# Kernel tuning notes

Measured on AMD Instinct MI355X. Metric: run time of the kernel, lower is better.

The kernel has to match this reference:

```python
import jax, jax.numpy as jnp
import numpy as np

D_IN, D_HID = 64, 128

def _ff(x, w1, b1, w2, b2):
    # FeedForward: Linear -> ReLU -> Linear
    return jax.nn.relu(x @ w1 + b1) @ w2 + b2

def setup_inputs() -> dict:
    key = jax.random.key(0)
    ks = jax.random.split(key, 10)
    N, m = 8, 2048
    def lin(k, fan_in, fan_out):
        bound = 1.0 / np.sqrt(fan_in)
        return jax.random.uniform(k, (fan_in, fan_out), jnp.float32, -bound, bound)
    return {
        "x": jax.random.normal(ks[0], (N, m, D_IN), jnp.float32),
        "edge": jax.random.uniform(ks[1], (N, m, m), jnp.float32),
        # f: dim_in -> dim_hid//2 -> dim_hid
        "f_w1": lin(ks[2], D_IN, D_HID // 2),
        "f_b1": jnp.zeros((D_HID // 2,), jnp.float32),
        "f_w2": lin(ks[3], D_HID // 2, D_HID),
        "f_b2": jnp.zeros((D_HID,), jnp.float32),
        # g: 2*dim_in -> dim_hid -> dim_hid
        "g_w1": lin(ks[4], 2 * D_IN, D_HID),
        "g_b1": jnp.zeros((D_HID,), jnp.float32),
        "g_w2": lin(ks[5], D_HID, D_HID),
        "g_b2": jnp.zeros((D_HID,), jnp.float32),
    }

def reference(x, edge, f_w1, f_b1, f_w2, f_b2, g_w1, g_b1, g_w2, g_b2):
    # self dynamics: f(x) -> [N, m, D_HID]
    self_dyn = _ff(x, f_w1, f_b1, f_w2, f_b2)
    # Original builds interaction[n,i,j] = cat(x[n,i], x[n,i]) (receiver is
    # transposed twice), so g is constant along j. Compute g once per sender node.
    gx = _ff(jnp.concatenate([x, x], axis=-1), g_w1, g_b1, g_w2, g_b2)  # [N, m, H]
    # interaction.sum over sender dim i with edge weights: out[n,j] = sum_i edge[n,i,j]*gx[n,i]
    inter = jnp.einsum('nij,nih->njh', edge, gx)
    return self_dyn + inter
```

## Files before the change

### kernel.cpp

```cpp
#include <hip/hip_runtime.h>


typedef __attribute__((ext_vector_type(8))) short bf16x8;
typedef __attribute__((ext_vector_type(8))) unsigned short u16x8;
typedef __attribute__((ext_vector_type(4))) unsigned short u16x4;
typedef __attribute__((ext_vector_type(4))) float f32x4;

static __device__ __forceinline__ unsigned short f2bf(float f) {
  union { float f; unsigned int i; } c; c.f = f;
  return (unsigned short)((c.i + 0x7fffu + ((c.i >> 16) & 1u)) >> 16);
}

__global__ __launch_bounds__(256) void k_self(
    const float* __restrict__ x,
    const float* __restrict__ fw1,
    const float* __restrict__ fb1,
    const float* __restrict__ fw2,
    const float* __restrict__ fb2,
    float* __restrict__ out)
{
  __shared__ short xs[64 * 64];
  __shared__ short w1T[64 * 64];
  __shared__ short w2T[128 * 64];
  __shared__ short h1s[64 * 64];

  const int t = threadIdx.x;
  const int R0 = blockIdx.x * 64;

  for (int idx = t; idx < 64 * 64; idx += 256) {
    int k = idx >> 6, n = idx & 63;
    w1T[(n << 6) + (((k >> 3) ^ (n & 7)) << 3) + (k & 7)] = (short)f2bf(fw1[idx]);
  }
  for (int idx = t; idx < 64 * 128; idx += 256) {
    int k = idx >> 7, n = idx & 127;
    w2T[(n << 6) + (((k >> 3) ^ (n & 7)) << 3) + (k & 7)] = (short)f2bf(fw2[idx]);
  }
  for (int s = t; s < 64 * 16; s += 256) {
    int row = s >> 4, c4 = s & 15;
    f32x4 v = *(const f32x4*)(x + (size_t)(R0 + row) * 64 + c4 * 4);
    u16x4 pk;
#pragma unroll
    for (int r = 0; r < 4; ++r) pk[r] = f2bf(v[r]);
    *(u16x4*)(xs + (row << 6) + (((c4 >> 1) ^ (row & 7)) << 3) + ((c4 & 1) << 2)) = pk;
  }
  __syncthreads();

  const int w = t >> 6, l = t & 63;
  const int lr = l & 15, q = l >> 4;
  const int mrow = w * 16 + lr;

  bf16x8 a[2];
#pragma unroll
  for (int ks = 0; ks < 2; ++ks) {
    int c = ks * 4 + q;
    a[ks] = *(const bf16x8*)(xs + (mrow << 6) + ((c ^ (mrow & 7)) << 3));
  }

  f32x4 acc;
#pragma unroll
  for (int nf = 0; nf < 4; ++nf) {
    acc = (f32x4){0.f, 0.f, 0.f, 0.f};
#pragma unroll
    for (int ks = 0; ks < 2; ++ks) {
      int c = ks * 4 + q;
      int nr = nf * 16 + lr;
      bf16x8 b = *(const bf16x8*)(w1T + (nr << 6) + ((c ^ (nr & 7)) << 3));
      acc = __builtin_amdgcn_mfma_f32_16x16x32_bf16(a[ks], b, acc, 0, 0, 0);
    }
    float bias = fb1[nf * 16 + lr];
#pragma unroll
    for (int r = 0; r < 4; ++r) {
      float v = acc[r] + bias;
      v = v > 0.f ? v : 0.f;
      int row = w * 16 + q * 4 + r, n = nf * 16 + lr;
      h1s[(row << 6) + (((n >> 3) ^ (row & 7)) << 3) + (n & 7)] = (short)f2bf(v);
    }
  }
  __syncthreads();

  bf16x8 a2[2];
#pragma unroll
  for (int ks = 0; ks < 2; ++ks) {
    int c = ks * 4 + q;
    a2[ks] = *(const bf16x8*)(h1s + (mrow << 6) + ((c ^ (mrow & 7)) << 3));
  }
#pragma unroll
  for (int nf = 0; nf < 8; ++nf) {
    acc = (f32x4){0.f, 0.f, 0.f, 0.f};
#pragma unroll
    for (int ks = 0; ks < 2; ++ks) {
      int c = ks * 4 + q;
      int nr = nf * 16 + lr;
      bf16x8 b = *(const bf16x8*)(w2T + (nr << 6) + ((c ^ (nr & 7)) << 3));
      acc = __builtin_amdgcn_mfma_f32_16x16x32_bf16(a2[ks], b, acc, 0, 0, 0);
    }
    float bias = fb2[nf * 16 + lr];
#pragma unroll
    for (int r = 0; r < 4; ++r)
      out[(size_t)(R0 + w * 16 + q * 4 + r) * 128 + nf * 16 + lr] = acc[r] + bias;
  }
}

__global__ __launch_bounds__(256) void k_gx(
    const float* __restrict__ x,
    const float* __restrict__ gw1,
    const float* __restrict__ gb1,
    const float* __restrict__ gw2,
    const float* __restrict__ gb2,
    unsigned short* __restrict__ gxT)
{
  __shared__ short xs[64 * 64];
  __shared__ short w1T[128 * 64];
  __shared__ short w2T[128 * 128];
  __shared__ short h2s[64 * 128];

  const int t = threadIdx.x;
  const int R0 = blockIdx.x * 64;

  for (int idx = t; idx < 64 * 128; idx += 256) {
    int k = idx >> 7, n = idx & 127;
    float v = gw1[idx] + gw1[64 * 128 + idx];
    w1T[(n << 6) + (((k >> 3) ^ (n & 7)) << 3) + (k & 7)] = (short)f2bf(v);
  }
  for (int idx = t; idx < 128 * 128; idx += 256) {
    int k = idx >> 7, n = idx & 127;
    w2T[(n << 7) + (((k >> 3) ^ (n & 7)) << 3) + (k & 7)] = (short)f2bf(gw2[idx]);
  }
  for (int s = t; s < 64 * 16; s += 256) {
    int row = s >> 4, c4 = s & 15;
    f32x4 v = *(const f32x4*)(x + (size_t)(R0 + row) * 64 + c4 * 4);
    u16x4 pk;
#pragma unroll
    for (int r = 0; r < 4; ++r) pk[r] = f2bf(v[r]);
    *(u16x4*)(xs + (row << 6) + (((c4 >> 1) ^ (row & 7)) << 3) + ((c4 & 1) << 2)) = pk;
  }
  __syncthreads();

  const int w = t >> 6, l = t & 63;
  const int lr = l & 15, q = l >> 4;
  const int mrow = w * 16 + lr;

  bf16x8 a[2];
#pragma unroll
  for (int ks = 0; ks < 2; ++ks) {
    int c = ks * 4 + q;
    a[ks] = *(const bf16x8*)(xs + (mrow << 6) + ((c ^ (mrow & 7)) << 3));
  }

  f32x4 acc;
#pragma unroll
  for (int nf = 0; nf < 8; ++nf) {
    acc = (f32x4){0.f, 0.f, 0.f, 0.f};
#pragma unroll
    for (int ks = 0; ks < 2; ++ks) {
      int c = ks * 4 + q;
      int nr = nf * 16 + lr;
      bf16x8 b = *(const bf16x8*)(w1T + (nr << 6) + ((c ^ (nr & 7)) << 3));
      acc = __builtin_amdgcn_mfma_f32_16x16x32_bf16(a[ks], b, acc, 0, 0, 0);
    }
    float bias = gb1[nf * 16 + lr];
#pragma unroll
    for (int r = 0; r < 4; ++r) {
      float v = acc[r] + bias;
      v = v > 0.f ? v : 0.f;
      int row = w * 16 + q * 4 + r, n = nf * 16 + lr;
      h2s[(row << 7) + (((n >> 3) ^ (row & 7)) << 3) + (n & 7)] = (short)f2bf(v);
    }
  }
  __syncthreads();

  bf16x8 a2[4];
#pragma unroll
  for (int ks = 0; ks < 4; ++ks) {
    int c = ks * 4 + q;
    a2[ks] = *(const bf16x8*)(h2s + (mrow << 7) + ((c ^ (mrow & 7)) << 3));
  }
  const int batch = R0 >> 11;
  const int ib = R0 & 2047;
#pragma unroll
  for (int nf = 0; nf < 8; ++nf) {
    acc = (f32x4){0.f, 0.f, 0.f, 0.f};
#pragma unroll
    for (int ks = 0; ks < 4; ++ks) {
      int c = ks * 4 + q;
      int nr = nf * 16 + lr;
      bf16x8 b = *(const bf16x8*)(w2T + (nr << 7) + ((c ^ (nr & 7)) << 3));
      acc = __builtin_amdgcn_mfma_f32_16x16x32_bf16(a2[ks], b, acc, 0, 0, 0);
    }
    float bias = gb2[nf * 16 + lr];
    u16x4 pk;
#pragma unroll
    for (int r = 0; r < 4; ++r) pk[r] = f2bf(acc[r] + bias);
    *(u16x4*)(gxT + (size_t)(batch * 128 + nf * 16 + lr) * 2048 + ib + w * 16 + q * 4) = pk;
  }
}

typedef __attribute__((ext_vector_type(8))) float f32x8;

__device__ __forceinline__ void load_tiles(const float* eb, const unsigned short* gb,
                                           int i0, int j0, int e_ii, int e_cj,
                                           f32x8 er[2], u16x8 gr[4])
{
  er[0] = *(const f32x8*)(eb + (size_t)(i0 + e_ii) * 2048 + j0 + e_cj * 8);
  er[1] = *(const f32x8*)(eb + (size_t)(i0 + e_ii + 32) * 2048 + j0 + e_cj * 8);
#pragma unroll
  for (int qq = 0; qq < 4; ++qq)
    gr[qq] = *(const u16x8*)(gb + (size_t)(qq * 32 + e_ii) * 2048 + i0 + e_cj * 8);
}

__global__ __launch_bounds__(256) void k_einsum(
    const float* __restrict__ edge,
    const unsigned short* __restrict__ gxT,
    float* __restrict__ out)
{
  __shared__ short eT[64 * 72];
  __shared__ short bT[128 * 64];

  const int t = threadIdx.x;
  const int batch = blockIdx.x & 7;
  const int jt = blockIdx.x >> 3;
  const int j0 = jt * 64;

  const int w = t >> 6, l = t & 63;
  const int wm = w & 1, wn = w >> 1;
  const int lr = l & 15, q = l >> 4;

  const float* eb = edge + (size_t)batch * 2048 * 2048;
  const unsigned short* gb = gxT + (size_t)batch * 128 * 2048;

  const int e_ii = t >> 3;
  const int e_cj = t & 7;

  f32x4 acc[2][4];
#pragma unroll
  for (int f = 0; f < 2; ++f)
#pragma unroll
    for (int nf = 0; nf < 4; ++nf) acc[f][nf] = (f32x4){0.f, 0.f, 0.f, 0.f};

  f32x8 er[2];
  u16x8 gr[4];
  load_tiles(eb, gb, 0, j0, e_ii, e_cj, er, gr);

  for (int kk = 0; kk < 32; ++kk) {
    __syncthreads();
#pragma unroll
    for (int rr = 0; rr < 2; ++rr) {
      int ii = e_ii + rr * 32;
#pragma unroll
      for (int u = 0; u < 8; ++u)
        eT[(e_cj * 8 + u) * 72 + (((ii >> 3) ^ e_cj) << 3) + (ii & 7)] = (short)f2bf(er[rr][u]);
    }
#pragma unroll
    for (int qq = 0; qq < 4; ++qq) {
      int r = qq * 32 + e_ii;
      *(u16x8*)(bT + (r << 6) + ((e_cj ^ (r & 7)) << 3)) = gr[qq];
    }
    __syncthreads();
    if (kk < 31) load_tiles(eb, gb, (kk + 1) * 64, j0, e_ii, e_cj, er, gr);

#pragma unroll
    for (int ks = 0; ks < 2; ++ks) {
      bf16x8 a[2], b[4];
#pragma unroll
      for (int f = 0; f < 2; ++f) {
        int jj = wm * 32 + f * 16 + lr;
        int c = ks * 4 + q;
        a[f] = *(const bf16x8*)(eT + jj * 72 + ((c ^ (jj >> 3)) << 3));
      }
#pragma unroll
      for (int nf = 0; nf < 4; ++nf) {
        int h = wn * 64 + nf * 16 + lr;
        int c = ks * 4 + q;
        b[nf] = *(const bf16x8*)(bT + (h << 6) + ((c ^ (h & 7)) << 3));
      }
#pragma unroll
      for (int f = 0; f < 2; ++f)
#pragma unroll
        for (int nf = 0; nf < 4; ++nf)
          acc[f][nf] = __builtin_amdgcn_mfma_f32_16x16x32_bf16(a[f], b[nf], acc[f][nf], 0, 0, 0);
    }
  }

  const size_t rowbase = (size_t)batch * 2048 + j0 + wm * 32;
#pragma unroll
  for (int f = 0; f < 2; ++f) {
#pragma unroll
    for (int nf = 0; nf < 4; ++nf) {
      int h = wn * 64 + nf * 16 + lr;
#pragma unroll
      for (int r = 0; r < 4; ++r) {
        size_t o = (rowbase + f * 16 + q * 4 + r) * 128 + h;
        out[o] = acc[f][nf][r] + out[o];
      }
    }
  }
}

extern "C" void kernel_launch(void* const* d_in, const int* in_sizes, int n_in,
                              void* d_out, int out_size, void* d_ws, size_t ws_size,
                              hipStream_t stream) {
  const float* x    = (const float*)d_in[0];
  const float* edge = (const float*)d_in[1];
  const float* fw1  = (const float*)d_in[2];
  const float* fb1  = (const float*)d_in[3];
  const float* fw2  = (const float*)d_in[4];
  const float* fb2  = (const float*)d_in[5];
  const float* gw1  = (const float*)d_in[6];
  const float* gb1  = (const float*)d_in[7];
  const float* gw2  = (const float*)d_in[8];
  const float* gb2  = (const float*)d_in[9];
  float* out = (float*)d_out;

  unsigned short* gxT = (unsigned short*)d_ws;

  hipLaunchKernelGGL(k_self, dim3(256), dim3(256), 0, stream, x, fw1, fb1, fw2, fb2, out);
  hipLaunchKernelGGL(k_gx, dim3(256), dim3(256), 0, stream, x, gw1, gb1, gw2, gb2, gxT);
  hipLaunchKernelGGL(k_einsum, dim3(256), dim3(256), 0, stream, edge, gxT, out);
}
```

Measured before the change: 243.7 us.

## Fuse self-dynamics MLP into einsum kernel and halve j-tile to 32

Removes the separate self-dynamics kernel and computes f(x) in the epilogue of the edge-weighted einsum kernel. The second layer accumulates directly into the einsum accumulators, so the out read-modify-write and one launch go away. The j-tile shrinks from 64 to 32 rows, doubling the grid to 512 blocks for better CU occupancy. The cost is that each block reloads the gxT tiles, roughly doubling gxT traffic, and converts the f weights once per block.

```diff
diff --git a/kernel.cpp b/kernel.cpp
--- a/kernel.cpp
+++ b/kernel.cpp
@@ -5,100 +5,11 @@
 typedef __attribute__((ext_vector_type(8))) unsigned short u16x8;
 typedef __attribute__((ext_vector_type(4))) unsigned short u16x4;
 typedef __attribute__((ext_vector_type(4))) float f32x4;
+typedef __attribute__((ext_vector_type(8))) float f32x8;
 
 static __device__ __forceinline__ unsigned short f2bf(float f) {
   union { float f; unsigned int i; } c; c.f = f;
   return (unsigned short)((c.i + 0x7fffu + ((c.i >> 16) & 1u)) >> 16);
-}
-
-__global__ __launch_bounds__(256) void k_self(
-    const float* __restrict__ x,
-    const float* __restrict__ fw1,
-    const float* __restrict__ fb1,
-    const float* __restrict__ fw2,
-    const float* __restrict__ fb2,
-    float* __restrict__ out)
-{
-  __shared__ short xs[64 * 64];
-  __shared__ short w1T[64 * 64];
-  __shared__ short w2T[128 * 64];
-  __shared__ short h1s[64 * 64];
-
-  const int t = threadIdx.x;
-  const int R0 = blockIdx.x * 64;
-
-  for (int idx = t; idx < 64 * 64; idx += 256) {
-    int k = idx >> 6, n = idx & 63;
-    w1T[(n << 6) + (((k >> 3) ^ (n & 7)) << 3) + (k & 7)] = (short)f2bf(fw1[idx]);
-  }
-  for (int idx = t; idx < 64 * 128; idx += 256) {
-    int k = idx >> 7, n = idx & 127;
-    w2T[(n << 6) + (((k >> 3) ^ (n & 7)) << 3) + (k & 7)] = (short)f2bf(fw2[idx]);
-  }
-  for (int s = t; s < 64 * 16; s += 256) {
-    int row = s >> 4, c4 = s & 15;
-    f32x4 v = *(const f32x4*)(x + (size_t)(R0 + row) * 64 + c4 * 4);
-    u16x4 pk;
-#pragma unroll
-    for (int r = 0; r < 4; ++r) pk[r] = f2bf(v[r]);
-    *(u16x4*)(xs + (row << 6) + (((c4 >> 1) ^ (row & 7)) << 3) + ((c4 & 1) << 2)) = pk;
-  }
-  __syncthreads();
-
-  const int w = t >> 6, l = t & 63;
-  const int lr = l & 15, q = l >> 4;
-  const int mrow = w * 16 + lr;
-
-  bf16x8 a[2];
-#pragma unroll
-  for (int ks = 0; ks < 2; ++ks) {
-    int c = ks * 4 + q;
-    a[ks] = *(const bf16x8*)(xs + (mrow << 6) + ((c ^ (mrow & 7)) << 3));
-  }
-
-  f32x4 acc;
-#pragma unroll
-  for (int nf = 0; nf < 4; ++nf) {
-    acc = (f32x4){0.f, 0.f, 0.f, 0.f};
-#pragma unroll
-    for (int ks = 0; ks < 2; ++ks) {
-      int c = ks * 4 + q;
-      int nr = nf * 16 + lr;
-      bf16x8 b = *(const bf16x8*)(w1T + (nr << 6) + ((c ^ (nr & 7)) << 3));
-      acc = __builtin_amdgcn_mfma_f32_16x16x32_bf16(a[ks], b, acc, 0, 0, 0);
-    }
-    float bias = fb1[nf * 16 + lr];
-#pragma unroll
-    for (int r = 0; r < 4; ++r) {
-      float v = acc[r] + bias;
-      v = v > 0.f ? v : 0.f;
-      int row = w * 16 + q * 4 + r, n = nf * 16 + lr;
-      h1s[(row << 6) + (((n >> 3) ^ (row & 7)) << 3) + (n & 7)] = (short)f2bf(v);
-    }
-  }
-  __syncthreads();
-
-  bf16x8 a2[2];
-#pragma unroll
-  for (int ks = 0; ks < 2; ++ks) {
-    int c = ks * 4 + q;
-    a2[ks] = *(const bf16x8*)(h1s + (mrow << 6) + ((c ^ (mrow & 7)) << 3));
-  }
-#pragma unroll
-  for (int nf = 0; nf < 8; ++nf) {
-    acc = (f32x4){0.f, 0.f, 0.f, 0.f};
-#pragma unroll
-    for (int ks = 0; ks < 2; ++ks) {
-      int c = ks * 4 + q;
-      int nr = nf * 16 + lr;
-      bf16x8 b = *(const bf16x8*)(w2T + (nr << 6) + ((c ^ (nr & 7)) << 3));
-      acc = __builtin_amdgcn_mfma_f32_16x16x32_bf16(a2[ks], b, acc, 0, 0, 0);
-    }
-    float bias = fb2[nf * 16 + lr];
-#pragma unroll
-    for (int r = 0; r < 4; ++r)
-      out[(size_t)(R0 + w * 16 + q * 4 + r) * 128 + nf * 16 + lr] = acc[r] + bias;
-  }
 }
 
 __global__ __launch_bounds__(256) void k_gx(
@@ -195,103 +106,157 @@
   }
 }
 
-typedef __attribute__((ext_vector_type(8))) float f32x8;
-
-__device__ __forceinline__ void load_tiles(const float* eb, const unsigned short* gb,
-                                           int i0, int j0, int e_ii, int e_cj,
-                                           f32x8 er[2], u16x8 gr[4])
+__device__ __forceinline__ void load_tiles(const float* ep, const unsigned short* gp,
+                                           f32x8& er, u16x8 gr[4])
 {
-  er[0] = *(const f32x8*)(eb + (size_t)(i0 + e_ii) * 2048 + j0 + e_cj * 8);
-  er[1] = *(const f32x8*)(eb + (size_t)(i0 + e_ii + 32) * 2048 + j0 + e_cj * 8);
+  er = *(const f32x8*)ep;
 #pragma unroll
   for (int qq = 0; qq < 4; ++qq)
-    gr[qq] = *(const u16x8*)(gb + (size_t)(qq * 32 + e_ii) * 2048 + i0 + e_cj * 8);
-}
-
-__global__ __launch_bounds__(256) void k_einsum(
+    gr[qq] = *(const u16x8*)(gp + (size_t)qq * 32 * 2048);
+}
+
+__global__ __launch_bounds__(256) void k_main(
     const float* __restrict__ edge,
     const unsigned short* __restrict__ gxT,
+    const float* __restrict__ x,
+    const float* __restrict__ fw1,
+    const float* __restrict__ fb1,
+    const float* __restrict__ fw2,
+    const float* __restrict__ fb2,
     float* __restrict__ out)
 {
-  __shared__ short eT[64 * 72];
+  __shared__ short eT[32 * 72];
   __shared__ short bT[128 * 64];
+  __shared__ short xs[32 * 64];
+  __shared__ short w1T[64 * 64];
+  __shared__ short h1s[32 * 64];
 
   const int t = threadIdx.x;
   const int batch = blockIdx.x & 7;
-  const int jt = blockIdx.x >> 3;
-  const int j0 = jt * 64;
+  const int j0 = (blockIdx.x >> 3) * 32;
 
   const int w = t >> 6, l = t & 63;
   const int wm = w & 1, wn = w >> 1;
   const int lr = l & 15, q = l >> 4;
 
-  const float* eb = edge + (size_t)batch * 2048 * 2048;
-  const unsigned short* gb = gxT + (size_t)batch * 128 * 2048;
-
-  const int e_ii = t >> 3;
-  const int e_cj = t & 7;
-
-  f32x4 acc[2][4];
-#pragma unroll
-  for (int f = 0; f < 2; ++f)
-#pragma unroll
-    for (int nf = 0; nf < 4; ++nf) acc[f][nf] = (f32x4){0.f, 0.f, 0.f, 0.f};
-
-  f32x8 er[2];
+  const int e_ii = t >> 2;
+  const int e_cj = t & 3;
+  const int g_hh = t >> 3;
+  const int g_ci = t & 7;
+
+  const float* ep = edge + (size_t)batch * 2048 * 2048 + (size_t)e_ii * 2048 + j0 + e_cj * 8;
+  const unsigned short* gp = gxT + (size_t)batch * 128 * 2048 + (size_t)g_hh * 2048 + g_ci * 8;
+
+  f32x4 acc[4];
+#pragma unroll
+  for (int nf = 0; nf < 4; ++nf) acc[nf] = (f32x4){0.f, 0.f, 0.f, 0.f};
+
+  f32x8 er;
   u16x8 gr[4];
-  load_tiles(eb, gb, 0, j0, e_ii, e_cj, er, gr);
+  load_tiles(ep, gp, er, gr);
 
   for (int kk = 0; kk < 32; ++kk) {
     __syncthreads();
 #pragma unroll
-    for (int rr = 0; rr < 2; ++rr) {
-      int ii = e_ii + rr * 32;
-#pragma unroll
-      for (int u = 0; u < 8; ++u)
-        eT[(e_cj * 8 + u) * 72 + (((ii >> 3) ^ e_cj) << 3) + (ii & 7)] = (short)f2bf(er[rr][u]);
-    }
+    for (int u = 0; u < 8; ++u)
+      eT[(e_cj * 8 + u) * 72 + (((e_ii >> 3) ^ e_cj) << 3) + (e_ii & 7)] = (short)f2bf(er[u]);
 #pragma unroll
     for (int qq = 0; qq < 4; ++qq) {
-      int r = qq * 32 + e_ii;
-      *(u16x8*)(bT + (r << 6) + ((e_cj ^ (r & 7)) << 3)) = gr[qq];
+      int r = qq * 32 + g_hh;
+      *(u16x8*)(bT + (r << 6) + ((g_ci ^ (r & 7)) << 3)) = gr[qq];
     }
     __syncthreads();
-    if (kk < 31) load_tiles(eb, gb, (kk + 1) * 64, j0, e_ii, e_cj, er, gr);
-
-#pragma unroll
-    for (int ks = 0; ks < 2; ++ks) {
-      bf16x8 a[2], b[4];
-#pragma unroll
-      for (int f = 0; f < 2; ++f) {
-        int jj = wm * 32 + f * 16 + lr;
-        int c = ks * 4 + q;
-        a[f] = *(const bf16x8*)(eT + jj * 72 + ((c ^ (jj >> 3)) << 3));
-      }
+    if (kk < 31) {
+      ep += 64 * 2048; gp += 64;
+      load_tiles(ep, gp, er, gr);
+    }
+
+#pragma unroll
+    for (int ks = 0; ks < 2; ++ks) {
+      const int c = ks * 4 + q;
+      const int jj = wm * 16 + lr;
+      bf16x8 a = *(const bf16x8*)(eT + jj * 72 + ((c ^ (jj >> 3)) << 3));
+      bf16x8 b[4];
 #pragma unroll
       for (int nf = 0; nf < 4; ++nf) {
         int h = wn * 64 + nf * 16 + lr;
-        int c = ks * 4 + q;
         b[nf] = *(const bf16x8*)(bT + (h << 6) + ((c ^ (h & 7)) << 3));
       }
 #pragma unroll
-      for (int f = 0; f < 2; ++f)
-#pragma unroll
-        for (int nf = 0; nf < 4; ++nf)
-          acc[f][nf] = __builtin_amdgcn_mfma_f32_16x16x32_bf16(a[f], b[nf], acc[f][nf], 0, 0, 0);
-    }
-  }
-
-  const size_t rowbase = (size_t)batch * 2048 + j0 + wm * 32;
-#pragma unroll
-  for (int f = 0; f < 2; ++f) {
+      for (int nf = 0; nf < 4; ++nf)
+        acc[nf] = __builtin_amdgcn_mfma_f32_16x16x32_bf16(a, b[nf], acc[nf], 0, 0, 0);
+    }
+  }
+
+  __syncthreads();
+  for (int idx = t; idx < 64 * 64; idx += 256) {
+    int k = idx >> 6, n = idx & 63;
+    w1T[(n << 6) + (((k >> 3) ^ (n & 7)) << 3) + (k & 7)] = (short)f2bf(fw1[idx]);
+  }
+  for (int idx = t; idx < 64 * 128; idx += 256) {
+    int k = idx >> 7, n = idx & 127;
+    bT[(n << 6) + (((k >> 3) ^ (n & 7)) << 3) + (k & 7)] = (short)f2bf(fw2[idx]);
+  }
+  for (int s = t; s < 32 * 16; s += 256) {
+    int row = s >> 4, c4 = s & 15;
+    f32x4 v = *(const f32x4*)(x + (size_t)(batch * 2048 + j0 + row) * 64 + c4 * 4);
+    u16x4 pk;
+#pragma unroll
+    for (int r = 0; r < 4; ++r) pk[r] = f2bf(v[r]);
+    *(u16x4*)(xs + (row << 6) + (((c4 >> 1) ^ (row & 7)) << 3) + ((c4 & 1) << 2)) = pk;
+  }
+  __syncthreads();
+
+  const int mrow = wm * 16 + lr;
+  if (wn == 0) {
+    bf16x8 a1[2];
+#pragma unroll
+    for (int ks = 0; ks < 2; ++ks) {
+      int c = ks * 4 + q;
+      a1[ks] = *(const bf16x8*)(xs + (mrow << 6) + ((c ^ (mrow & 7)) << 3));
+    }
 #pragma unroll
     for (int nf = 0; nf < 4; ++nf) {
-      int h = wn * 64 + nf * 16 + lr;
+      f32x4 h = (f32x4){0.f, 0.f, 0.f, 0.f};
+#pragma unroll
+      for (int ks = 0; ks < 2; ++ks) {
+        int c = ks * 4 + q;
+        int nr = nf * 16 + lr;
+        bf16x8 b = *(const bf16x8*)(w1T + (nr << 6) + ((c ^ (nr & 7)) << 3));
+        h = __builtin_amdgcn_mfma_f32_16x16x32_bf16(a1[ks], b, h, 0, 0, 0);
+      }
+      float bias = fb1[nf * 16 + lr];
 #pragma unroll
       for (int r = 0; r < 4; ++r) {
-        size_t o = (rowbase + f * 16 + q * 4 + r) * 128 + h;
-        out[o] = acc[f][nf][r] + out[o];
+        float v = h[r] + bias;
+        v = v > 0.f ? v : 0.f;
+        int row = wm * 16 + q * 4 + r, n = nf * 16 + lr;
+        h1s[(row << 6) + (((n >> 3) ^ (row & 7)) << 3) + (n & 7)] = (short)f2bf(v);
       }
+    }
+  }
+  __syncthreads();
+
+  bf16x8 a2[2];
+#pragma unroll
+  for (int ks = 0; ks < 2; ++ks) {
+    int c = ks * 4 + q;
+    a2[ks] = *(const bf16x8*)(h1s + (mrow << 6) + ((c ^ (mrow & 7)) << 3));
+  }
+#pragma unroll
+  for (int nf = 0; nf < 4; ++nf) {
+    int h = wn * 64 + nf * 16 + lr;
+#pragma unroll
+    for (int ks = 0; ks < 2; ++ks) {
+      int c = ks * 4 + q;
+      bf16x8 b = *(const bf16x8*)(bT + (h << 6) + ((c ^ (h & 7)) << 3));
+      acc[nf] = __builtin_amdgcn_mfma_f32_16x16x32_bf16(a2[ks], b, acc[nf], 0, 0, 0);
+    }
+    float bias = fb2[h];
+#pragma unroll
+    for (int r = 0; r < 4; ++r) {
+      size_t o = ((size_t)batch * 2048 + j0 + wm * 16 + q * 4 + r) * 128 + h;
+      out[o] = acc[nf][r] + bias;
     }
   }
 }
@@ -313,7 +278,7 @@
 
   unsigned short* gxT = (unsigned short*)d_ws;
 
-  hipLaunchKernelGGL(k_self, dim3(256), dim3(256), 0, stream, x, fw1, fb1, fw2, fb2, out);
   hipLaunchKernelGGL(k_gx, dim3(256), dim3(256), 0, stream, x, gw1, gb1, gw2, gb2, gxT);
-  hipLaunchKernelGGL(k_einsum, dim3(256), dim3(256), 0, stream, edge, gxT, out);
-}
+  hipLaunchKernelGGL(k_main, dim3(512), dim3(256), 0, stream, edge, gxT, x,
+                     fw1, fb1, fw2, fb2, out);
+}
```

New measurement: 239.6 us. About the same (-1.7%).
